# Kernel tuning notes

Hardware: AMD Instinct MI355X
Metric: run time of the kernel (lower is better)

## Reference

```python
import jax, jax.numpy as jnp
import numpy as np

B, S, H, NH = 4, 2048, 768, 12
PH = H // NH  # per-head size


def setup_inputs() -> dict:
    key = jax.random.key(0)
    ks = jax.random.split(key, 12)
    s = 0.02
    return {
        "key": jax.random.normal(ks[0], (B, S, H), jnp.float32),
        "value": jax.random.normal(ks[1], (B, S, H), jnp.float32),
        "query": jax.random.normal(ks[2], (B, S, H), jnp.float32),
        "mask": jnp.zeros((B, 1, S, S), jnp.float32),  # additive mask
        "Wq": jax.random.normal(ks[3], (H, H), jnp.float32) * s,
        "bq": jnp.zeros((H,), jnp.float32),
        "Wk": jax.random.normal(ks[4], (H, H), jnp.float32) * s,
        "bk": jnp.zeros((H,), jnp.float32),
        "Wv": jax.random.normal(ks[5], (H, H), jnp.float32) * s,
        "bv": jnp.zeros((H,), jnp.float32),
        "Wo": jax.random.normal(ks[6], (H, H), jnp.float32) * s,
        "bo": jnp.zeros((H,), jnp.float32),
    }


def _heads(x):
    # [B,S,H] -> [B,NH,S,PH]
    return x.reshape(B, S, NH, PH).transpose(0, 2, 1, 3)


def reference(key, value, query, mask, Wq, bq, Wk, bk, Wv, bv, Wo, bo):
    # torch Linear: y = x @ W.T + b  (separate projections for q, k, v)
    q = _heads(query @ Wq.T + bq)
    k = _heads(key @ Wk.T + bk)
    v = _heads(value @ Wv.T + bv)
    scale = 1.0 / jnp.sqrt(jnp.asarray(PH, q.dtype))
    scores = jnp.einsum("bhqd,bhkd->bhqk", q, k) * scale + mask
    probs = jax.nn.softmax(scores, axis=-1)  # dropout p=0 -> identity
    out = jnp.einsum("bhqk,bhkd->bhqd", probs, v)
    out = out.transpose(0, 2, 1, 3).reshape(B, S, H)
    return out @ Wo.T + bo
```

## Files before the change

kernel.cpp:

```cpp
#include <hip/hip_runtime.h>
#include <hip/hip_bf16.h>
#include <cstddef>
#include <cstdint>

#define BB  4
#define SS  2048
#define HH  768
#define NHH 12
#define PHH 64
#define MM  (BB*SS)
#define LOG2E 1.4426950408889634f

typedef short         short8   __attribute__((ext_vector_type(8)));
typedef float         floatx4  __attribute__((ext_vector_type(4)));
typedef float         floatx16 __attribute__((ext_vector_type(16)));
typedef unsigned int  uint4v   __attribute__((ext_vector_type(4)));

static __device__ __forceinline__ unsigned short f2bf(float f) {
    unsigned int u = __float_as_uint(f);
    u += 0x7FFF + ((u >> 16) & 1);
    return (unsigned short)(u >> 16);
}

static __device__ __forceinline__ unsigned int cvtpk_bf16(float lo, float hi) {
    unsigned int r;
    asm("v_cvt_pk_bf16_f32 %0, %1, %2" : "=v"(r) : "v"(lo), "v"(hi));
    return r;
}

static __device__ __forceinline__ float v_exp2(float x) {
    float r;
    asm("v_exp_f32 %0, %1" : "=v"(r) : "v"(x));
    return r;
}

static __device__ __forceinline__ void plswap(unsigned int& a, unsigned int& b) {
    asm("v_permlane32_swap_b32 %0, %1" : "+v"(a), "+v"(b));
}

static __device__ __forceinline__ short8 mk_short8(unsigned int a, unsigned int b,
                                                   unsigned int c, unsigned int d) {
    uint4v u = {a, b, c, d};
    return __builtin_bit_cast(short8, u);
}

#define GLOAD_LDS16(g, l) __builtin_amdgcn_global_load_lds(            \
        (const __attribute__((address_space(1))) void*)(g),            \
        (__attribute__((address_space(3))) void*)(l), 16, 0, 0)

#define MFMA32(a, b, c) __builtin_amdgcn_mfma_f32_32x32x16_bf16((a), (b), (c), 0, 0, 0)

__global__ void mha_prep(const float* __restrict__ w0, const float* __restrict__ w1,
                         const float* __restrict__ w2, const float* __restrict__ w3,
                         unsigned short* __restrict__ dst,
                         const float* __restrict__ mask,
                         unsigned char* __restrict__ flags8) {
    const int bid = blockIdx.x;
    const int t = threadIdx.x;
    if (bid < 2304) {
        const int i = bid * 256 + t;
        const int which = i / 147456;
        const int j = i - which * 147456;
        const float* s = (which == 0) ? w0 : (which == 1) ? w1 : (which == 2) ? w2 : w3;
        float4 v = reinterpret_cast<const float4*>(s)[j];
        unsigned long long pk =
            (unsigned long long)f2bf(v.x)         |
            ((unsigned long long)f2bf(v.y) << 16) |
            ((unsigned long long)f2bf(v.z) << 32) |
            ((unsigned long long)f2bf(v.w) << 48);
        reinterpret_cast<unsigned long long*>(dst)[i] = pk;
    } else {
        const int fb = bid - 2304;
        const int b  = fb >> 10;
        const int rem = fb & 1023;
        const int qt = rem >> 5;
        const int kt = rem & 31;
        const float* base = mask + ((size_t)b*SS + (size_t)qt*64)*SS + kt*64;
        const int lrow = t >> 4;
        const int lcol = (t & 15) * 4;
        int nz = 0;
        #pragma unroll
        for (int i = 0; i < 4; ++i) {
            float4 v = *reinterpret_cast<const float4*>(base + (size_t)(lrow + 16*i)*SS + lcol);
            nz |= (v.x != 0.f) | (v.y != 0.f) | (v.z != 0.f) | (v.w != 0.f);
        }
        __shared__ int s;
        if (t == 0) s = 0;
        __syncthreads();
        if (nz) s = 1;
        __syncthreads();
        if (t == 0) flags8[fb] = (unsigned char)s;
    }
}

template<int AIN_F32, int MODE>
__global__ __launch_bounds__(256) void mha_gemm(
        const void* __restrict__ Xv,
        const unsigned short* __restrict__ W,
        const float* __restrict__ bias,
        void* __restrict__ out) {
    __shared__ unsigned short As[2][64 * 64];
    __shared__ unsigned short Bs[2][128 * 64];
    const int wave = threadIdx.x >> 6;
    const int lane = threadIdx.x & 63;
    const int lq = lane & 15, lg = lane >> 4;
    const int m0 = blockIdx.x * 64;
    const int n0 = blockIdx.y * 128;
    const int brow = lane >> 3;
    const int bcol = 8 * (lane & 7);
    const int srow = lane >> 2;
    const int scol = 16 * (lane & 3);

    const float* Xr32 = (const float*)Xv + (size_t)(m0 + wave*16 + srow)*HH + scol;

#define STAGE_B(bi, k0)                                                        \
    {                                                                          \
        _Pragma("unroll")                                                      \
        for (int c = 0; c < 4; ++c) {                                          \
            const int ch = 4*wave + c;                                         \
            GLOAD_LDS16(W + (size_t)(n0 + ch*8 + brow)*HH + (k0) + bcol,       \
                        &Bs[bi][ch*512]);                                      \
        }                                                                      \
    }
#define STAGE_A16(bi, k0)                                                      \
    {                                                                          \
        _Pragma("unroll")                                                      \
        for (int c = 0; c < 2; ++c) {                                          \
            const int ch = 2*wave + c;                                         \
            GLOAD_LDS16((const unsigned short*)Xv                              \
                            + (size_t)(m0 + ch*8 + brow)*HH + (k0) + bcol,     \
                        &As[bi][ch*512]);                                      \
        }                                                                      \
    }

    floatx4 acc[4][2];
    #pragma unroll
    for (int m = 0; m < 4; ++m)
        #pragma unroll
        for (int n = 0; n < 2; ++n) acc[m][n] = (floatx4){0.f, 0.f, 0.f, 0.f};

    float4 a0, a1, a2, a3;
    if constexpr (AIN_F32) {
        a0 = *reinterpret_cast<const float4*>(Xr32);
        a1 = *reinterpret_cast<const float4*>(Xr32 + 4);
        a2 = *reinterpret_cast<const float4*>(Xr32 + 8);
        a3 = *reinterpret_cast<const float4*>(Xr32 + 12);
    } else {
        STAGE_A16(0, 0)
    }
    STAGE_B(0, 0)

    #pragma unroll 1
    for (int t = 0; t < 12; ++t) {
        const int cur = t & 1, nxt = cur ^ 1;
        const int kN = ((t + 1) % 12) * 64;

        if constexpr (AIN_F32) {
            unsigned short* aw = &As[cur][(wave*16 + srow)*64 + scol];
            uint4v u0 = { cvtpk_bf16(a0.x, a0.y), cvtpk_bf16(a0.z, a0.w),
                          cvtpk_bf16(a1.x, a1.y), cvtpk_bf16(a1.z, a1.w) };
            uint4v u1 = { cvtpk_bf16(a2.x, a2.y), cvtpk_bf16(a2.z, a2.w),
                          cvtpk_bf16(a3.x, a3.y), cvtpk_bf16(a3.z, a3.w) };
            *reinterpret_cast<uint4v*>(aw) = u0;
            *reinterpret_cast<uint4v*>(aw + 8) = u1;
            a0 = *reinterpret_cast<const float4*>(Xr32 + kN);
            a1 = *reinterpret_cast<const float4*>(Xr32 + kN + 4);
            a2 = *reinterpret_cast<const float4*>(Xr32 + kN + 8);
            a3 = *reinterpret_cast<const float4*>(Xr32 + kN + 12);
            STAGE_B(nxt, kN)
            asm volatile("s_waitcnt vmcnt(8) lgkmcnt(0)" ::: "memory");
        } else {
            STAGE_A16(nxt, kN)
            STAGE_B(nxt, kN)
            asm volatile("s_waitcnt vmcnt(6)" ::: "memory");
        }
        __builtin_amdgcn_sched_barrier(0);
        __builtin_amdgcn_s_barrier();

        short8 af[4][2], bw[2][2];
        #pragma unroll
        for (int m = 0; m < 4; ++m)
            #pragma unroll
            for (int kk = 0; kk < 2; ++kk)
                af[m][kk] = *reinterpret_cast<const short8*>(
                                &As[cur][(16*m + lq)*64 + 32*kk + 8*lg]);
        #pragma unroll
        for (int n = 0; n < 2; ++n)
            #pragma unroll
            for (int kk = 0; kk < 2; ++kk)
                bw[n][kk] = *reinterpret_cast<const short8*>(
                                &Bs[cur][(32*wave + 16*n + lq)*64 + 32*kk + 8*lg]);
        #pragma unroll
        for (int kk = 0; kk < 2; ++kk)
            #pragma unroll
            for (int m = 0; m < 4; ++m)
                #pragma unroll
                for (int n = 0; n < 2; ++n)
                    acc[m][n] = __builtin_amdgcn_mfma_f32_16x16x32_bf16(
                                    af[m][kk], bw[n][kk], acc[m][n], 0, 0, 0);

        asm volatile("s_waitcnt lgkmcnt(0)" ::: "memory");
        __builtin_amdgcn_sched_barrier(0);
        __builtin_amdgcn_s_barrier();
    }
#undef STAGE_B
#undef STAGE_A16

    #pragma unroll
    for (int n = 0; n < 2; ++n) {
        const int col = n0 + wave*32 + 16*n + lq;
        const float bv = bias[col];
        #pragma unroll
        for (int m = 0; m < 4; ++m) {
            #pragma unroll
            for (int r = 0; r < 4; ++r) {
                const int row = m0 + 16*m + 4*lg + r;
                float y = acc[m][n][r] + bv;
                if constexpr (MODE == 1) {
                    ((unsigned short*)out)[(size_t)row*HH + col] = f2bf(y * (0.125f * LOG2E));
                } else if constexpr (MODE == 3) {
                    ((float*)out)[(size_t)row*HH + col] = y;
                } else if constexpr (MODE == 4) {
                    int bb = row >> 11, s = row & 2047;
                    int hh = col >> 6,  d = col & 63;
                    int kt = s >> 6, half = (s >> 5) & 1, rr = s & 31;
                    int ks = d >> 4, h2 = (d >> 3) & 1, j = d & 7;
                    size_t idx = (((size_t)(bb*NHH + hh)*32 + kt)*4096)
                               + (half*4 + ks)*512 + (h2*32 + rr)*8 + j;
                    ((unsigned short*)out)[idx] = f2bf(y);
                } else {
                    int bb = row >> 11, s = row & 2047;
                    int hh = col >> 6,  d = col & 63;
                    int kt = s >> 6, ss = s & 63;
                    int ks = ss >> 4, h2 = (ss >> 3) & 1, j = ss & 7;
                    int vh = d >> 5, qq = d & 31;
                    size_t idx = (((size_t)(bb*NHH + hh)*32 + kt)*4096)
                               + (vh*4 + ks)*512 + (h2*32 + qq)*8 + j;
                    ((unsigned short*)out)[idx] = f2bf(y);
                }
            }
        }
    }
}

__global__ __launch_bounds__(256, 3) void mha_attn(
        const unsigned short* __restrict__ qb,
        const unsigned short* __restrict__ kfb,
        const unsigned short* __restrict__ vfb,
        const float* __restrict__ mask,
        const unsigned char* __restrict__ flags8,
        unsigned short* __restrict__ ab) {
    __shared__ unsigned short ldsbuf[2][8192];

    const int wave = threadIdx.x >> 6;
    const int lane = threadIdx.x & 63;
    const int ql   = lane & 31;
    const int hi   = lane >> 5;

    int bid = blockIdx.x;
    bid = (bid & 7) * 96 + (bid >> 3);
    const int qblk = bid & 15;
    int t = bid >> 4;
    const int h = t % NHH;
    const int b = t / NHH;

    const int q0 = qblk*128 + wave*32;
    const int q  = q0 + ql;

    const unsigned short* qp = qb + ((size_t)b*SS + q)*HH + h*PHH + 8*hi;
    short8 qf[4];
    #pragma unroll
    for (int ks = 0; ks < 4; ++ks)
        qf[ks] = *reinterpret_cast<const short8*>(qp + 16*ks);

    short8 ones;
    #pragma unroll
    for (int i = 0; i < 8; ++i) ones[i] = (short)0x3F80;

    const unsigned short* kvK = kfb + (size_t)(b*NHH + h) * 32 * 4096;
    const unsigned short* kvV = vfb + (size_t)(b*NHH + h) * 32 * 4096;
    const float* mrow = mask + ((size_t)b*SS + q)*SS;

    unsigned int fm = 0;
    {
        const unsigned int* fw = (const unsigned int*)(flags8 + b*1024 + (q0 >> 6)*32);
        #pragma unroll
        for (int i = 0; i < 8; ++i) {
            unsigned int w = fw[i];
            fm |= ((w & 1u) << (4*i))       | (((w >> 8) & 1u) << (4*i + 1))
                | (((w >> 16) & 1u) << (4*i + 2)) | (((w >> 24) & 1u) << (4*i + 3));
        }
    }

    floatx16 o0, o1, lacc;
    #pragma unroll
    for (int i = 0; i < 16; ++i) { o0[i] = 0.f; o1[i] = 0.f; lacc[i] = 0.f; }

#define STAGE(bufi, kti)                                                       \
    {                                                                          \
        _Pragma("unroll")                                                      \
        for (int c = 0; c < 4; ++c) {                                          \
            const int ch = 4*wave + c;                                         \
            const unsigned short* src = (ch < 8)                               \
                ? (kvK + (size_t)(kti)*4096 + ch*512)                          \
                : (kvV + (size_t)(kti)*4096 + (ch - 8)*512);                   \
            GLOAD_LDS16(src + lane*8, &ldsbuf[bufi][ch*512]);                  \
        }                                                                      \
    }

    STAGE(0, 0)

    #pragma unroll 1
    for (int kt = 0; kt < 32; ++kt) {
        const int cur = kt & 1;
        STAGE(cur ^ 1, (kt + 1) & 31)

        asm volatile("s_waitcnt vmcnt(4)" ::: "memory");
        __builtin_amdgcn_sched_barrier(0);
        __builtin_amdgcn_s_barrier();

        const unsigned short* lk = &ldsbuf[cur][0];

        short8 kf[8];
        #pragma unroll
        for (int f = 0; f < 8; ++f)
            kf[f] = *reinterpret_cast<const short8*>(lk + f*512 + lane*8);
        floatx16 s0, s1;
        #pragma unroll
        for (int i = 0; i < 16; ++i) { s0[i] = 0.f; s1[i] = 0.f; }
        __builtin_amdgcn_s_setprio(1);
        #pragma unroll
        for (int ks = 0; ks < 4; ++ks) {
            s0 = MFMA32(kf[ks],   qf[ks], s0);
            s1 = MFMA32(kf[4+ks], qf[ks], s1);
        }
        __builtin_amdgcn_s_setprio(0);

        if (fm & (1u << kt)) {
            const float* mr = mrow + kt*64;
            #pragma unroll
            for (int g = 0; g < 4; ++g) {
                float4 a = *reinterpret_cast<const float4*>(mr + 8*g + 4*hi);
                float4 c = *reinterpret_cast<const float4*>(mr + 32 + 8*g + 4*hi);
                s0[4*g+0] = fmaf(a.x, LOG2E, s0[4*g+0]);
                s0[4*g+1] = fmaf(a.y, LOG2E, s0[4*g+1]);
                s0[4*g+2] = fmaf(a.z, LOG2E, s0[4*g+2]);
                s0[4*g+3] = fmaf(a.w, LOG2E, s0[4*g+3]);
                s1[4*g+0] = fmaf(c.x, LOG2E, s1[4*g+0]);
                s1[4*g+1] = fmaf(c.y, LOG2E, s1[4*g+1]);
                s1[4*g+2] = fmaf(c.z, LOG2E, s1[4*g+2]);
                s1[4*g+3] = fmaf(c.w, LOG2E, s1[4*g+3]);
            }
        }

        #pragma unroll
        for (int r = 0; r < 16; ++r) s0[r] = v_exp2(s0[r]);
        #pragma unroll
        for (int r = 0; r < 16; ++r) s1[r] = v_exp2(s1[r]);

        unsigned int c0 = cvtpk_bf16(s0[0],  s0[1]),  c1 = cvtpk_bf16(s0[2],  s0[3]);
        unsigned int c2 = cvtpk_bf16(s0[4],  s0[5]),  c3 = cvtpk_bf16(s0[6],  s0[7]);
        unsigned int c4 = cvtpk_bf16(s0[8],  s0[9]),  c5 = cvtpk_bf16(s0[10], s0[11]);
        unsigned int c6 = cvtpk_bf16(s0[12], s0[13]), c7 = cvtpk_bf16(s0[14], s0[15]);
        unsigned int d0 = cvtpk_bf16(s1[0],  s1[1]),  d1 = cvtpk_bf16(s1[2],  s1[3]);
        unsigned int d2 = cvtpk_bf16(s1[4],  s1[5]),  d3 = cvtpk_bf16(s1[6],  s1[7]);
        unsigned int d4 = cvtpk_bf16(s1[8],  s1[9]),  d5 = cvtpk_bf16(s1[10], s1[11]);
        unsigned int d6 = cvtpk_bf16(s1[12], s1[13]), d7 = cvtpk_bf16(s1[14], s1[15]);
        plswap(c0, c2); plswap(c1, c3); plswap(c4, c6); plswap(c5, c7);
        plswap(d0, d2); plswap(d1, d3); plswap(d4, d6); plswap(d5, d7);
        short8 pa[4];
        pa[0] = mk_short8(c0, c1, c2, c3);
        pa[1] = mk_short8(c4, c5, c6, c7);
        pa[2] = mk_short8(d0, d1, d2, d3);
        pa[3] = mk_short8(d4, d5, d6, d7);

        const unsigned short* lv = lk + 4096;
        short8 vf[8];
        #pragma unroll
        for (int g = 0; g < 8; ++g)
            vf[g] = *reinterpret_cast<const short8*>(lv + g*512 + lane*8);
        __builtin_amdgcn_s_setprio(1);
        #pragma unroll
        for (int ks = 0; ks < 4; ++ks) {
            o0   = MFMA32(vf[ks],   pa[ks], o0);
            o1   = MFMA32(vf[4+ks], pa[ks], o1);
            lacc = MFMA32(ones,     pa[ks], lacc);
        }
        __builtin_amdgcn_s_setprio(0);

        asm volatile("s_waitcnt lgkmcnt(0)" ::: "memory");
        __builtin_amdgcn_sched_barrier(0);
        __builtin_amdgcn_s_barrier();
    }
#undef STAGE

    const float inv = 1.f / lacc[0];
    unsigned short* op = ab + ((size_t)b*SS + q)*HH + h*PHH + 4*hi;
    #pragma unroll
    for (int g = 0; g < 4; ++g) {
        ushort4 w0, w1;
        w0.x = f2bf(o0[4*g+0]*inv); w0.y = f2bf(o0[4*g+1]*inv);
        w0.z = f2bf(o0[4*g+2]*inv); w0.w = f2bf(o0[4*g+3]*inv);
        w1.x = f2bf(o1[4*g+0]*inv); w1.y = f2bf(o1[4*g+1]*inv);
        w1.z = f2bf(o1[4*g+2]*inv); w1.w = f2bf(o1[4*g+3]*inv);
        *reinterpret_cast<ushort4*>(op + 8*g)      = w0;
        *reinterpret_cast<ushort4*>(op + 32 + 8*g) = w1;
    }
}

extern "C" void kernel_launch(void* const* d_in, const int* in_sizes, int n_in,
                              void* d_out, int out_size, void* d_ws, size_t ws_size,
                              hipStream_t stream) {
    const float* key   = (const float*)d_in[0];
    const float* value = (const float*)d_in[1];
    const float* query = (const float*)d_in[2];
    const float* mask  = (const float*)d_in[3];
    const float* Wq    = (const float*)d_in[4];
    const float* bq    = (const float*)d_in[5];
    const float* Wk    = (const float*)d_in[6];
    const float* bk    = (const float*)d_in[7];
    const float* Wv    = (const float*)d_in[8];
    const float* bv    = (const float*)d_in[9];
    const float* Wo    = (const float*)d_in[10];
    const float* bo    = (const float*)d_in[11];
    float* out = (float*)d_out;

    const size_t WSZ = (size_t)HH * HH;
    const size_t ASZ = (size_t)MM * HH;
    unsigned short* wqb = (unsigned short*)d_ws;
    unsigned short* wkb = wqb + WSZ;
    unsigned short* wvb = wkb + WSZ;
    unsigned short* wob = wvb + WSZ;
    unsigned short* qb  = wob + WSZ;
    unsigned short* kfb = qb + ASZ;
    unsigned short* vfb = kfb + ASZ;
    unsigned short* xb  = vfb + ASZ;
    unsigned char* flags8 = (unsigned char*)(xb + ASZ);

    mha_prep<<<2304 + 4096, 256, 0, stream>>>(Wq, Wk, Wv, Wo, wqb, mask, flags8);

    dim3 g(MM/64, HH/128);
    mha_gemm<1,1><<<g, 256, 0, stream>>>(query, wqb, bq, qb);
    mha_gemm<1,4><<<g, 256, 0, stream>>>(key,   wkb, bk, kfb);
    mha_gemm<1,5><<<g, 256, 0, stream>>>(value, wvb, bv, vfb);

    mha_attn<<<BB*NHH*(SS/128), 256, 0, stream>>>(qb, kfb, vfb, mask, flags8, xb);

    mha_gemm<0,3><<<g, 256, 0, stream>>>(xb, wob, bo, out);
}
```

Before: 174.7 us.

## Triple-buffer attention KV tiles and simplify projection GEMM to single buffer

The attention kernel's K/V LDS staging moves from a double to a triple buffer ring, allowing the trailing per-iteration barrier to be removed. The projection GEMM drops its double-buffered software pipeline in favour of a single LDS buffer with plain __syncthreads around each k-step. The attention change aims to cut barrier stalls. The GEMM change removes overlap of global loads with MFMA work and raises LDS use in attention, which may lower occupancy.

```diff
diff --git a/kernel.cpp b/kernel.cpp
--- a/kernel.cpp
+++ b/kernel.cpp
@@ -99,8 +99,8 @@
         const unsigned short* __restrict__ W,
         const float* __restrict__ bias,
         void* __restrict__ out) {
-    __shared__ unsigned short As[2][64 * 64];
-    __shared__ unsigned short Bs[2][128 * 64];
+    __shared__ unsigned short As[64 * 64];
+    __shared__ unsigned short Bs[128 * 64];
     const int wave = threadIdx.x >> 6;
     const int lane = threadIdx.x & 63;
     const int lq = lane & 15, lg = lane >> 4;
@@ -112,26 +112,7 @@
     const int scol = 16 * (lane & 3);
 
     const float* Xr32 = (const float*)Xv + (size_t)(m0 + wave*16 + srow)*HH + scol;
-
-#define STAGE_B(bi, k0)                                                        \
-    {                                                                          \
-        _Pragma("unroll")                                                      \
-        for (int c = 0; c < 4; ++c) {                                          \
-            const int ch = 4*wave + c;                                         \
-            GLOAD_LDS16(W + (size_t)(n0 + ch*8 + brow)*HH + (k0) + bcol,       \
-                        &Bs[bi][ch*512]);                                      \
-        }                                                                      \
-    }
-#define STAGE_A16(bi, k0)                                                      \
-    {                                                                          \
-        _Pragma("unroll")                                                      \
-        for (int c = 0; c < 2; ++c) {                                          \
-            const int ch = 2*wave + c;                                         \
-            GLOAD_LDS16((const unsigned short*)Xv                              \
-                            + (size_t)(m0 + ch*8 + brow)*HH + (k0) + bcol,     \
-                        &As[bi][ch*512]);                                      \
-        }                                                                      \
-    }
+    unsigned short* As_w = As + (wave*16 + srow)*64 + scol;
 
     floatx4 acc[4][2];
     #pragma unroll
@@ -139,57 +120,46 @@
         #pragma unroll
         for (int n = 0; n < 2; ++n) acc[m][n] = (floatx4){0.f, 0.f, 0.f, 0.f};
 
-    float4 a0, a1, a2, a3;
-    if constexpr (AIN_F32) {
-        a0 = *reinterpret_cast<const float4*>(Xr32);
-        a1 = *reinterpret_cast<const float4*>(Xr32 + 4);
-        a2 = *reinterpret_cast<const float4*>(Xr32 + 8);
-        a3 = *reinterpret_cast<const float4*>(Xr32 + 12);
-    } else {
-        STAGE_A16(0, 0)
-    }
-    STAGE_B(0, 0)
-
-    #pragma unroll 1
-    for (int t = 0; t < 12; ++t) {
-        const int cur = t & 1, nxt = cur ^ 1;
-        const int kN = ((t + 1) % 12) * 64;
-
+    for (int k0 = 0; k0 < HH; k0 += 64) {
+        #pragma unroll
+        for (int c = 0; c < 4; ++c) {
+            const int ch = 4*wave + c;
+            GLOAD_LDS16(W + (size_t)(n0 + ch*8 + brow)*HH + k0 + bcol, Bs + ch*512);
+        }
         if constexpr (AIN_F32) {
-            unsigned short* aw = &As[cur][(wave*16 + srow)*64 + scol];
+            float4 a0 = *reinterpret_cast<const float4*>(Xr32 + k0);
+            float4 a1 = *reinterpret_cast<const float4*>(Xr32 + k0 + 4);
+            float4 a2 = *reinterpret_cast<const float4*>(Xr32 + k0 + 8);
+            float4 a3 = *reinterpret_cast<const float4*>(Xr32 + k0 + 12);
             uint4v u0 = { cvtpk_bf16(a0.x, a0.y), cvtpk_bf16(a0.z, a0.w),
                           cvtpk_bf16(a1.x, a1.y), cvtpk_bf16(a1.z, a1.w) };
             uint4v u1 = { cvtpk_bf16(a2.x, a2.y), cvtpk_bf16(a2.z, a2.w),
                           cvtpk_bf16(a3.x, a3.y), cvtpk_bf16(a3.z, a3.w) };
-            *reinterpret_cast<uint4v*>(aw) = u0;
-            *reinterpret_cast<uint4v*>(aw + 8) = u1;
-            a0 = *reinterpret_cast<const float4*>(Xr32 + kN);
-            a1 = *reinterpret_cast<const float4*>(Xr32 + kN + 4);
-            a2 = *reinterpret_cast<const float4*>(Xr32 + kN + 8);
-            a3 = *reinterpret_cast<const float4*>(Xr32 + kN + 12);
-            STAGE_B(nxt, kN)
-            asm volatile("s_waitcnt vmcnt(8) lgkmcnt(0)" ::: "memory");
+            *reinterpret_cast<uint4v*>(As_w) = u0;
+            *reinterpret_cast<uint4v*>(As_w + 8) = u1;
         } else {
-            STAGE_A16(nxt, kN)
-            STAGE_B(nxt, kN)
-            asm volatile("s_waitcnt vmcnt(6)" ::: "memory");
-        }
-        __builtin_amdgcn_sched_barrier(0);
-        __builtin_amdgcn_s_barrier();
-
+            #pragma unroll
+            for (int c = 0; c < 2; ++c) {
+                const int ch = 2*wave + c;
+                GLOAD_LDS16((const unsigned short*)Xv
+                                + (size_t)(m0 + ch*8 + brow)*HH + k0 + bcol,
+                            As + ch*512);
+            }
+        }
+        __syncthreads();
         short8 af[4][2], bw[2][2];
         #pragma unroll
         for (int m = 0; m < 4; ++m)
             #pragma unroll
             for (int kk = 0; kk < 2; ++kk)
                 af[m][kk] = *reinterpret_cast<const short8*>(
-                                &As[cur][(16*m + lq)*64 + 32*kk + 8*lg]);
+                                As + (16*m + lq)*64 + 32*kk + 8*lg);
         #pragma unroll
         for (int n = 0; n < 2; ++n)
             #pragma unroll
             for (int kk = 0; kk < 2; ++kk)
                 bw[n][kk] = *reinterpret_cast<const short8*>(
-                                &Bs[cur][(32*wave + 16*n + lq)*64 + 32*kk + 8*lg]);
+                                Bs + (32*wave + 16*n + lq)*64 + 32*kk + 8*lg);
         #pragma unroll
         for (int kk = 0; kk < 2; ++kk)
             #pragma unroll
@@ -198,13 +168,8 @@
                 for (int n = 0; n < 2; ++n)
                     acc[m][n] = __builtin_amdgcn_mfma_f32_16x16x32_bf16(
                                     af[m][kk], bw[n][kk], acc[m][n], 0, 0, 0);
-
-        asm volatile("s_waitcnt lgkmcnt(0)" ::: "memory");
-        __builtin_amdgcn_sched_barrier(0);
-        __builtin_amdgcn_s_barrier();
-    }
-#undef STAGE_B
-#undef STAGE_A16
+        __syncthreads();
+    }
 
     #pragma unroll
     for (int n = 0; n < 2; ++n) {
@@ -250,7 +215,7 @@
         const float* __restrict__ mask,
         const unsigned char* __restrict__ flags8,
         unsigned short* __restrict__ ab) {
-    __shared__ unsigned short ldsbuf[2][8192];
+    __shared__ unsigned short ldsbuf[3][8192];
 
     const int wave = threadIdx.x >> 6;
     const int lane = threadIdx.x & 63;
@@ -312,8 +277,8 @@
 
     #pragma unroll 1
     for (int kt = 0; kt < 32; ++kt) {
-        const int cur = kt & 1;
-        STAGE(cur ^ 1, (kt + 1) & 31)
+        const int cur = kt % 3;
+        STAGE((kt + 1) % 3, (kt + 1) & 31)
 
         asm volatile("s_waitcnt vmcnt(4)" ::: "memory");
         __builtin_amdgcn_sched_barrier(0);
@@ -387,10 +352,6 @@
             lacc = MFMA32(ones,     pa[ks], lacc);
         }
         __builtin_amdgcn_s_setprio(0);
-
-        asm volatile("s_waitcnt lgkmcnt(0)" ::: "memory");
-        __builtin_amdgcn_sched_barrier(0);
-        __builtin_amdgcn_s_barrier();
     }
 #undef STAGE
 
```

After: 164.8 us (median of 3 runs). 1.06x faster.
